# Performance work log

Hardware: AMD Instinct MI355X
Metric: run time of the kernel (lower is better)

## Reference

```python
import jax, jax.numpy as jnp
import numpy as np

B, K, H, T, V = 32, 5, 512, 256, 5000
MAX_LEN = 64
SOS, EOS, PAD = 1, 2, 0
NEG = -1e9
ALPHA, MIN_LEN = 1.2, 5.0
SCALE = 1.0 / float(np.sqrt(H))


def setup_inputs() -> dict:
    key = jax.random.key(0)
    ks = jax.random.split(key, 5)
    s = 0.02
    return {
        "input_var": jnp.full((B, 1), SOS, dtype=jnp.int32),
        "encoder_outputs": jax.random.normal(ks[0], (B, T, H), dtype=jnp.float32),
        "emb_table": jax.random.normal(ks[1], (V, H), dtype=jnp.float32) * s,
        "w_ih": jax.random.normal(ks[2], (H, 3 * H), dtype=jnp.float32) * s,
        "w_hh": jax.random.normal(ks[3], (H, 3 * H), dtype=jnp.float32) * s,
        "w_out": jax.random.normal(ks[4], (2 * H, V), dtype=jnp.float32) * s,
        "k": K,
    }


def _gru_cell(x, h, w_ih, w_hh):
    iz, ir, inn = jnp.split(x @ w_ih, 3, axis=-1)
    hz, hr, hn = jnp.split(h @ w_hh, 3, axis=-1)
    z = jax.nn.sigmoid(iz + hz)
    r = jax.nn.sigmoid(ir + hr)
    n = jnp.tanh(inn + r * hn)
    return (1.0 - z) * n + z * h


def _forward_step(tok, h, enc, emb_table, w_ih, w_hh, w_out):
    # tok: [N] int, h: [N,H], enc: [N,T,H] -> (log-probs [N,V], new hidden [N,H])
    x = emb_table[tok]
    h = _gru_cell(x, h, w_ih, w_hh)
    att = jax.nn.softmax(jnp.einsum("nh,nth->nt", h, enc) * SCALE, axis=-1)
    ctx = jnp.einsum("nt,nth->nh", att, enc)
    logits = jnp.concatenate([h, ctx], axis=-1) @ w_out
    return jax.nn.log_softmax(logits, axis=-1), h


def reference(input_var, encoder_outputs, emb_table, w_ih, w_hh, w_out, k):
    bsz = encoder_outputs.shape[0]
    f32 = encoder_outputs.dtype

    # --- first step on un-inflated batch (hidden starts at zeros) ---
    h0 = jnp.zeros((bsz, H), dtype=f32)
    lp0, h1 = _forward_step(input_var[:, 0], h0, encoder_outputs,
                            emb_table, w_ih, w_hh, w_out)
    cum, beams = jax.lax.top_k(lp0, k)            # [B,k], [B,k]

    # inflate encoder states / hidden to beam-major layout [B*k, ...]
    enc_k = jnp.repeat(encoder_outputs, k, axis=0)   # [B*k,T,H]
    h = jnp.repeat(h1, k, axis=0)                    # [B*k,H]

    tokens = jnp.zeros((bsz, k, MAX_LEN), dtype=jnp.int32)
    tokens = tokens.at[:, :, 0].set(beams)
    finished = beams == EOS
    lengths = jnp.ones((bsz, k), dtype=jnp.int32)
    # finished beams may only extend with PAD at zero added log-prob
    pad_lp = jnp.where(jnp.arange(V) == PAD, 0.0, NEG).astype(f32)

    def body(carry, di):
        tokens, last, cum, h, finished, lengths = carry
        lp, h_new = _forward_step(last.reshape(-1), h, enc_k,
                                  emb_table, w_ih, w_hh, w_out)
        lp = lp.reshape(bsz, k, V)
        lp = jnp.where(finished[:, :, None], pad_lp[None, None, :], lp)
        # joint top-k over k*V candidates == per-beam topk(k) then topk over k^2
        cand = (cum[:, :, None] + lp).reshape(bsz, k * V)
        scores, idx = jax.lax.top_k(cand, k)      # [B,k]
        beam_ids = idx // V
        tok_ids = idx % V
        tokens = jnp.take_along_axis(tokens, beam_ids[:, :, None], axis=1)
        tokens = tokens.at[:, :, di].set(tok_ids)
        prev_fin = jnp.take_along_axis(finished, beam_ids, axis=1)
        lengths = jnp.take_along_axis(lengths, beam_ids, axis=1) + jnp.where(prev_fin, 0, 1)
        finished = prev_fin | (tok_ids == EOS)
        h = jnp.take_along_axis(h_new.reshape(bsz, k, H),
                                beam_ids[:, :, None], axis=1).reshape(bsz * k, H)
        return (tokens, tok_ids, scores, h, finished, lengths), None

    carry = (tokens, beams.astype(jnp.int32), cum, h, finished, lengths)
    (tokens, _, cum, _, finished, lengths), _ = jax.lax.scan(
        body, carry, jnp.arange(1, MAX_LEN))

    # length penalty on finished hypotheses, then pick best beam per batch
    penalty = ((MIN_LEN + lengths.astype(f32)) / (MIN_LEN + 1.0)) ** ALPHA
    sel = jnp.where(finished, cum / penalty, cum)
    best = jnp.argmax(sel, axis=1)
    hypothesis = jnp.take_along_axis(tokens, best[:, None, None], axis=1)[:, 0, :]
    return hypothesis, cum
```

## Files before the change

### kernel.cpp

```cpp
#include <hip/hip_runtime.h>
#include <math.h>

#define BB     32
#define KBM    5
#define NR     160
#define HD     512
#define TT     256
#define VV     5000
#define MAXLEN 64
#define EOSID  2
#define NEGV   (-1e9f)
#define NEGBIG (-3.0e38f)
#define SCALEF 0.04419417382415922f
#define NBLK   256
#define NTHR   512

typedef float v4f __attribute__((ext_vector_type(4)));

__device__ __forceinline__ float ld_sysf(const float* p) {
  return __hip_atomic_load(p, __ATOMIC_RELAXED, __HIP_MEMORY_SCOPE_SYSTEM);
}
__device__ __forceinline__ void st_sysf(float* p, float v) {
  __hip_atomic_store(p, v, __ATOMIC_RELAXED, __HIP_MEMORY_SCOPE_SYSTEM);
}
__device__ __forceinline__ int ld_sysi(const int* p) {
  return __hip_atomic_load(p, __ATOMIC_RELAXED, __HIP_MEMORY_SCOPE_SYSTEM);
}
__device__ __forceinline__ void st_sysi(int* p, int v) {
  __hip_atomic_store(p, v, __ATOMIC_RELAXED, __HIP_MEMORY_SCOPE_SYSTEM);
}

__device__ __forceinline__ v4f ld4_issue_sys(const float* p) {
  v4f v;
  asm volatile("global_load_dwordx4 %0, %1, off sc0 sc1" : "=v"(v) : "v"(p));
  return v;
}
__device__ __forceinline__ v4f ld4_issue(const float* p) {
  v4f v;
  asm volatile("global_load_dwordx4 %0, %1, off" : "=v"(v) : "v"(p));
  return v;
}
__device__ __forceinline__ void vm_bind2(v4f& a, v4f& b) {
  asm volatile("s_waitcnt vmcnt(0)" : "+v"(a), "+v"(b) :: "memory");
}
__device__ __forceinline__ void vm_bind3(v4f& a, v4f& b, v4f& c) {
  asm volatile("s_waitcnt vmcnt(0)" : "+v"(a), "+v"(b), "+v"(c) :: "memory");
}
__device__ __forceinline__ void vm_bind4(v4f& a, v4f& b, v4f& c, v4f& d) {
  asm volatile("s_waitcnt vmcnt(0)" : "+v"(a), "+v"(b), "+v"(c), "+v"(d) :: "memory");
}
__device__ __forceinline__ void vm_bind5(v4f& a, v4f& b, v4f& c, v4f& d, v4f& e) {
  asm volatile("s_waitcnt vmcnt(0)"
               : "+v"(a), "+v"(b), "+v"(c), "+v"(d), "+v"(e) :: "memory");
}
__device__ __forceinline__ void st4_sys(float* p, v4f v) {
  asm volatile("global_store_dwordx4 %0, %1, off sc0 sc1" :: "v"(p), "v"(v) : "memory");
}

__device__ __forceinline__ bool viBetter(float av, int ai, float bv, int bi) {
  return (av > bv) || (av == bv && ai < bi);
}

__device__ __forceinline__ void top5_insert(float tv[5], int ti[5], float x, int v) {
  if (!viBetter(x, v, tv[4], ti[4])) return;
  tv[4] = x; ti[4] = v;
#pragma unroll
  for (int q = 4; q > 0; q--) {
    if (viBetter(tv[q], ti[q], tv[q - 1], ti[q - 1])) {
      float tf = tv[q - 1]; int tx2 = ti[q - 1];
      tv[q - 1] = tv[q]; ti[q - 1] = ti[q];
      tv[q] = tf; ti[q] = tx2;
    } else break;
  }
}

template<int LEVELS>
__device__ __forceinline__ void bfly_argmax(float& v, int& i) {
#pragma unroll
  for (int d = 1; d < (1 << LEVELS); d <<= 1) {
    float ov = __shfl_xor(v, d);
    int oi = __shfl_xor(i, d);
    if (viBetter(ov, oi, v, i)) { v = ov; i = oi; }
  }
}

__global__ void k_zero(unsigned int* bar) {
  if (threadIdx.x < 320)
    __hip_atomic_store(&bar[threadIdx.x], 0u, __ATOMIC_RELAXED, __HIP_MEMORY_SCOPE_SYSTEM);
}

__launch_bounds__(NTHR, 1)
__global__ void k_persist(const int* __restrict__ input_var, const float* __restrict__ enc,
                          const float* __restrict__ emb, const float* __restrict__ w_ih,
                          const float* __restrict__ w_hh, const float* __restrict__ w_out,
                          float* __restrict__ out,
                          float* h, float* A_cat, float* summ,
                          int* last_tok, unsigned int* bar) {
  const int bid = blockIdx.x;
  const int tid = threadIdx.x;
  unsigned int ep = 0;

  __shared__ float sh_xs[32][40];
  __shared__ float sh_hs[32][40];
  __shared__ float sh_ws[6][32][32];
  __shared__ int   sh_toks[32];
  __shared__ float sh_h5[KBM][HD];
  __shared__ float sh_part[2][KBM][TT];
  __shared__ float sh_sc5[KBM][TT];
  __shared__ float sh_tmp5[KBM][TT];
  __shared__ float sh_as[32][72];
  __shared__ float sh_bs[64][136];
  __shared__ float sh_candV[KBM * KBM]; __shared__ int sh_candI[KBM * KBM];
  __shared__ int   sh_tokens[KBM][MAXLEN];
  __shared__ float sh_cum[KBM];
  __shared__ int   sh_fin[KBM]; __shared__ int sh_len[KBM];
  __shared__ float sh_oc[KBM];  __shared__ int sh_ofin[KBM]; __shared__ int sh_olen[KBM];
  __shared__ int   sh_ttmp[KBM * MAXLEN];
  __shared__ int   sh_selI[KBM]; __shared__ float sh_selV[KBM];

  auto gbar = [&]() {
    asm volatile("s_waitcnt vmcnt(0)" ::: "memory");
    __syncthreads();
    ep += 1;
    if (tid == 0) {
      __hip_atomic_fetch_add(&bar[(bid & 7) * 32], 1u, __ATOMIC_RELAXED,
                             __HIP_MEMORY_SCOPE_SYSTEM);
      if (bid == 0) {
        for (int c = 0; c < 8; c++) {
          while (__hip_atomic_load(&bar[c * 32], __ATOMIC_RELAXED,
                                   __HIP_MEMORY_SCOPE_SYSTEM) < ep * 32u) {
            __builtin_amdgcn_s_sleep(1);
          }
        }
        __hip_atomic_store(&bar[288], ep, __ATOMIC_RELAXED, __HIP_MEMORY_SCOPE_SYSTEM);
      } else {
        while (__hip_atomic_load(&bar[288], __ATOMIC_RELAXED,
                                 __HIP_MEMORY_SCOPE_SYSTEM) < ep) {
          __builtin_amdgcn_s_sleep(2);
        }
      }
    }
    __syncthreads();
  };

  if (bid < BB) {
    if (tid < KBM) { sh_cum[tid] = 0.f; sh_fin[tid] = 0; sh_len[tid] = 0; }
    for (int t = tid; t < KBM * MAXLEN; t += NTHR) sh_tokens[t >> 6][t & 63] = 0;
  }
  {
    int gidx = bid * NTHR + tid;
    v4f z4; z4[0] = z4[1] = z4[2] = z4[3] = 0.f;
    for (int i = gidx; i < NR * HD / 4; i += NBLK * NTHR) st4_sys(&h[i * 4], z4);
    for (int t = gidx; t < NR; t += NBLK * NTHR) st_sysi(&last_tok[t], input_var[t / KBM]);
  }
  gbar();

  for (int di = 0; di < MAXLEN; di++) {
    if (bid < 80) {
      const int bx = bid & 15, by = bid >> 4;
      const int i0 = bx * 32, n0 = by * 32;
      const int tx = tid & 31, ty = tid >> 5;
      if (tid < 32) sh_toks[tid] = ld_sysi(&last_tok[n0 + tid]);
      float acc[6][2];
#pragma unroll
      for (int g = 0; g < 6; g++) { acc[g][0] = 0.f; acc[g][1] = 0.f; }
      float hcap0 = 0.f, hcap1 = 0.f;

      for (int k0 = 0; k0 < HD; k0 += 32) {
        __syncthreads();
        v4f v0, v1, v2, v3;
        if (tid < 256) {
          int r = tid >> 3, c4 = (tid & 7) * 4;
          v0 = ld4_issue(&emb[(size_t)sh_toks[r] * HD + k0 + c4]);
        } else {
          int r = (tid - 256) >> 3, c4 = ((tid - 256) & 7) * 4;
          v0 = ld4_issue_sys(&h[(size_t)(n0 + r) * HD + k0 + c4]);
        }
        int gW[3], kW[3], cW[3];
#pragma unroll
        for (int p = 0; p < 3; p++) {
          int widx = tid + p * 512;
          int g = widx >> 8, rem = widx & 255;
          int kk = rem >> 3, c4 = (rem & 7) * 4;
          const float* W = (g < 3) ? w_ih : w_hh;
          int gc = (g < 3) ? g : g - 3;
          v4f t = ld4_issue(&W[(size_t)(k0 + kk) * 1536 + gc * HD + i0 + c4]);
          if (p == 0) v1 = t; else if (p == 1) v2 = t; else v3 = t;
          gW[p] = g; kW[p] = kk; cW[p] = c4;
        }
        vm_bind4(v0, v1, v2, v3);
        if (tid < 256) {
          int r = tid >> 3, c4 = (tid & 7) * 4;
          *(v4f*)&sh_xs[r][c4] = v0;
        } else {
          int r = (tid - 256) >> 3, c4 = ((tid - 256) & 7) * 4;
          *(v4f*)&sh_hs[r][c4] = v0;
        }
        *(v4f*)&sh_ws[gW[0]][kW[0]][cW[0]] = v1;
        *(v4f*)&sh_ws[gW[1]][kW[1]][cW[1]] = v2;
        *(v4f*)&sh_ws[gW[2]][kW[2]][cW[2]] = v3;
        __syncthreads();
        if (k0 == i0) {
          hcap0 = sh_hs[ty * 2 + 0][tx];
          hcap1 = sh_hs[ty * 2 + 1][tx];
        }
#pragma unroll 8
        for (int k = 0; k < 32; k++) {
          float w0 = sh_ws[0][k][tx], w1 = sh_ws[1][k][tx], w2 = sh_ws[2][k][tx];
          float w3 = sh_ws[3][k][tx], w4 = sh_ws[4][k][tx], w5 = sh_ws[5][k][tx];
#pragma unroll
          for (int rr = 0; rr < 2; rr++) {
            float xv = sh_xs[ty * 2 + rr][k];
            float hv = sh_hs[ty * 2 + rr][k];
            acc[0][rr] += xv * w0; acc[1][rr] += xv * w1; acc[2][rr] += xv * w2;
            acc[3][rr] += hv * w3; acc[4][rr] += hv * w4; acc[5][rr] += hv * w5;
          }
        }
      }
#pragma unroll
      for (int rr = 0; rr < 2; rr++) {
        int n = n0 + ty * 2 + rr, i = i0 + tx;
        float hv = rr ? hcap1 : hcap0;
        float z = 1.f / (1.f + expf(-(acc[0][rr] + acc[3][rr])));
        float r = 1.f / (1.f + expf(-(acc[1][rr] + acc[4][rr])));
        float nn = tanhf(acc[2][rr] + r * acc[5][rr]);
        st_sysf(&A_cat[(size_t)n * 1024 + i], (1.f - z) * nn + z * hv);
      }
    }
    gbar();

    if (bid < BB) {
      const int b = bid;
      {
        v4f x0, x1 = {};
        int j0 = tid >> 7, kc0 = (tid & 127) * 4;
        x0 = ld4_issue_sys(&A_cat[(size_t)(b * KBM + j0) * 1024 + kc0]);
        if (tid < 128) {
          int idx = tid + 512;
          x1 = ld4_issue_sys(&A_cat[(size_t)(b * KBM + (idx >> 7)) * 1024 + (idx & 127) * 4]);
        }
        vm_bind2(x0, x1);
        *(v4f*)&sh_h5[j0][kc0] = x0;
        if (tid < 128) {
          int idx = tid + 512;
          *(v4f*)&sh_h5[idx >> 7][(idx & 127) * 4] = x1;
        }
      }
      __syncthreads();
      {
        const int t = tid & 255, half = tid >> 8;
        const int kb = half * 256;
        float a[KBM];
#pragma unroll
        for (int j = 0; j < KBM; j++) a[j] = 0.f;
        const float* ep2 = enc + ((size_t)b * TT + t) * HD + kb;
#pragma unroll 4
        for (int k = 0; k < 256; k += 4) {
          v4f e = *(const v4f*)(ep2 + k);
#pragma unroll
          for (int j = 0; j < KBM; j++) {
            v4f hj = *(const v4f*)&sh_h5[j][kb + k];
            a[j] += hj[0] * e[0] + hj[1] * e[1] + hj[2] * e[2] + hj[3] * e[3];
          }
        }
#pragma unroll
        for (int j = 0; j < KBM; j++) sh_part[half][j][t] = a[j];
      }
      __syncthreads();
      if (tid < 256) {
#pragma unroll
        for (int j = 0; j < KBM; j++) {
          float sc = (sh_part[0][j][tid] + sh_part[1][j][tid]) * SCALEF;
          sh_sc5[j][tid] = sc;
          sh_tmp5[j][tid] = sc;
        }
      }
      __syncthreads();
      for (int off = 128; off > 0; off >>= 1) {
        if (tid < off) {
#pragma unroll
          for (int j = 0; j < KBM; j++)
            sh_tmp5[j][tid] = fmaxf(sh_tmp5[j][tid], sh_tmp5[j][tid + off]);
        }
        __syncthreads();
      }
      float mj[KBM];
#pragma unroll
      for (int j = 0; j < KBM; j++) mj[j] = sh_tmp5[j][0];
      __syncthreads();
      if (tid < 256) {
#pragma unroll
        for (int j = 0; j < KBM; j++) {
          float e = expf(sh_sc5[j][tid] - mj[j]);
          sh_sc5[j][tid] = e;
          sh_tmp5[j][tid] = e;
        }
      }
      __syncthreads();
      for (int off = 128; off > 0; off >>= 1) {
        if (tid < off) {
#pragma unroll
          for (int j = 0; j < KBM; j++) sh_tmp5[j][tid] += sh_tmp5[j][tid + off];
        }
        __syncthreads();
      }
      float Sj[KBM];
#pragma unroll
      for (int j = 0; j < KBM; j++) Sj[j] = sh_tmp5[j][0];
      __syncthreads();
      if (tid < 256) {
#pragma unroll
        for (int j = 0; j < KBM; j++) sh_sc5[j][tid] = sh_sc5[j][tid] / Sj[j];
      }
      __syncthreads();
      {
        float cx[KBM];
#pragma unroll
        for (int j = 0; j < KBM; j++) cx[j] = 0.f;
        const float* eb = enc + (size_t)b * TT * HD + tid;
#pragma unroll 8
        for (int t2 = 0; t2 < TT; t2++) {
          float e = eb[(size_t)t2 * HD];
#pragma unroll
          for (int j = 0; j < KBM; j++) cx[j] += sh_sc5[j][t2] * e;
        }
#pragma unroll
        for (int j = 0; j < KBM; j++)
          st_sysf(&A_cat[(size_t)(b * KBM + j) * 1024 + HD + tid], cx[j]);
      }
    }
    gbar();

    if (bid < 200) {
      const int bc = bid % 40, br = bid / 40;
      const int c0 = bc * 128, n0 = br * 32;
      const int tx = tid & 31, ty = tid >> 5;
      float acc[2][4];
#pragma unroll
      for (int rr = 0; rr < 2; rr++)
#pragma unroll
        for (int cc = 0; cc < 4; cc++) acc[rr][cc] = 0.f;

      for (int k0 = 0; k0 < 1024; k0 += 64) {
        __syncthreads();
        v4f a0, b0, b1, b2, b3;
        const int ar = tid >> 4, ak4 = (tid & 15) * 4;
        a0 = ld4_issue_sys(&A_cat[(size_t)(n0 + ar) * 1024 + k0 + ak4]);
        int kkB[4], cB[4];
#pragma unroll
        for (int p = 0; p < 4; p++) {
          int idx = tid + p * 512;
          int kk = idx >> 5, c4 = (idx & 31) * 4;
          int col = c0 + c4;
          v4f t; t[0] = t[1] = t[2] = t[3] = 0.f;
          if (col + 3 < VV) t = ld4_issue(&w_out[(size_t)(k0 + kk) * VV + col]);
          if (p == 0) b0 = t; else if (p == 1) b1 = t; else if (p == 2) b2 = t; else b3 = t;
          kkB[p] = kk; cB[p] = c4;
        }
        vm_bind5(a0, b0, b1, b2, b3);
        *(v4f*)&sh_as[ar][ak4] = a0;
        *(v4f*)&sh_bs[kkB[0]][cB[0]] = b0;
        *(v4f*)&sh_bs[kkB[1]][cB[1]] = b1;
        *(v4f*)&sh_bs[kkB[2]][cB[2]] = b2;
        *(v4f*)&sh_bs[kkB[3]][cB[3]] = b3;
        __syncthreads();
#pragma unroll 16
        for (int k = 0; k < 64; k++) {
          v4f bv = *(const v4f*)&sh_bs[k][tx * 4];
#pragma unroll
          for (int rr = 0; rr < 2; rr++) {
            float a = sh_as[ty * 2 + rr][k];
            acc[rr][0] += a * bv[0]; acc[rr][1] += a * bv[1];
            acc[rr][2] += a * bv[2]; acc[rr][3] += a * bv[3];
          }
        }
      }
#pragma unroll
      for (int rr = 0; rr < 2; rr++) {
        const int rowg = n0 + ty * 2 + rr;
        float vv[4]; int ci[4];
        float m = NEGBIG, s = 0.f;
#pragma unroll
        for (int cc = 0; cc < 4; cc++) {
          int c = c0 + tx * 4 + cc;
          ci[cc] = c;
          if (c < VV) {
            float x = acc[rr][cc];
            vv[cc] = x;
            float mn = fmaxf(m, x);
            s = s * expf(m - mn) + expf(x - mn);
            m = mn;
          } else {
            vv[cc] = NEGBIG;
          }
        }
#pragma unroll
        for (int d = 1; d < 32; d <<= 1) {
          float om = __shfl_xor(m, d), os = __shfl_xor(s, d);
          float mm = fmaxf(m, om);
          s = s * expf(m - mm) + os * expf(om - mm);
          m = mm;
        }
        float tv[5]; int ti[5];
#pragma unroll
        for (int q = 0; q < 5; q++) {
          float bvv = vv[0]; int bii = ci[0];
#pragma unroll
          for (int cc = 1; cc < 4; cc++)
            if (viBetter(vv[cc], ci[cc], bvv, bii)) { bvv = vv[cc]; bii = ci[cc]; }
          bfly_argmax<5>(bvv, bii);
          tv[q] = bvv; ti[q] = bii;
#pragma unroll
          for (int cc = 0; cc < 4; cc++)
            if (ci[cc] == bii) vv[cc] = -3.2e38f;
        }
        if ((tid & 31) == 0) {
          float* base = &summ[((size_t)rowg * 40 + bc) * 12];
          v4f p0v, p1v, p2v;
          p0v[0] = m; p0v[1] = s; p0v[2] = tv[0]; p0v[3] = tv[1];
          p1v[0] = tv[2]; p1v[1] = tv[3]; p1v[2] = tv[4];
          p1v[3] = __int_as_float(ti[0]);
          p2v[0] = __int_as_float(ti[1]); p2v[1] = __int_as_float(ti[2]);
          p2v[2] = __int_as_float(ti[3]); p2v[3] = __int_as_float(ti[4]);
          st4_sys(base, p0v); st4_sys(base + 4, p1v); st4_sys(base + 8, p2v);
        }
      }
    }
    gbar();

    if (bid < BB) {
      const int b = bid;
      if (tid < KBM) {
        sh_oc[tid] = sh_cum[tid]; sh_ofin[tid] = sh_fin[tid]; sh_olen[tid] = sh_len[tid];
      }
      for (int t = tid; t < KBM * MAXLEN; t += NTHR) sh_ttmp[t] = sh_tokens[t >> 6][t & 63];
      __syncthreads();

      const int w = tid >> 6, lane = tid & 63;
      const bool act = (di == 0) ? (w == 0) : (w < KBM);
      if (act) {
        const int j = (di == 0) ? 0 : w;
        if (di > 0 && sh_ofin[j]) {
          if (lane == 0) {
            float cj = sh_oc[j];
            sh_candV[j * KBM + 0] = cj;
            sh_candI[j * KBM + 0] = j * VV + 0;
#pragma unroll
            for (int q = 1; q < KBM; q++) {
              sh_candV[j * KBM + q] = cj + NEGV;
              sh_candI[j * KBM + q] = j * VV + q;
            }
          }
        } else {
          const int row = b * KBM + j;
          float m, s; float lv[5]; int li[5];
          if (lane < 40) {
            const float* base = &summ[((size_t)row * 40 + lane) * 12];
            v4f s0 = ld4_issue_sys(base);
            v4f s1 = ld4_issue_sys(base + 4);
            v4f s2 = ld4_issue_sys(base + 8);
            vm_bind3(s0, s1, s2);
            m = s0[0]; s = s0[1];
            lv[0] = s0[2]; lv[1] = s0[3]; lv[2] = s1[0]; lv[3] = s1[1]; lv[4] = s1[2];
            li[0] = __float_as_int(s1[3]);
            li[1] = __float_as_int(s2[0]); li[2] = __float_as_int(s2[1]);
            li[3] = __float_as_int(s2[2]); li[4] = __float_as_int(s2[3]);
          } else {
            m = NEGBIG; s = 0.f;
#pragma unroll
            for (int q = 0; q < 5; q++) { lv[q] = NEGBIG; li[q] = 0x7fffffff; }
          }
#pragma unroll
          for (int d = 1; d < 64; d <<= 1) {
            float om = __shfl_xor(m, d), os = __shfl_xor(s, d);
            float mm = fmaxf(m, om);
            s = s * expf(m - mm) + os * expf(om - mm);
            m = mm;
          }
          float lse = m + logf(s);
          float cj = (di == 0) ? 0.f : sh_oc[j];
#pragma unroll
          for (int q = 0; q < 5; q++) {
            float bvv = lv[0]; int bii = li[0];
#pragma unroll
            for (int p = 1; p < 5; p++)
              if (viBetter(lv[p], li[p], bvv, bii)) { bvv = lv[p]; bii = li[p]; }
            bfly_argmax<6>(bvv, bii);
            if (lane == 0) {
              sh_candV[j * KBM + q] = cj + (bvv - lse);
              sh_candI[j * KBM + q] = j * VV + bii;
            }
#pragma unroll
            for (int p = 0; p < 5; p++)
              if (li[p] == bii) lv[p] = -3.2e38f;
          }
        }
      }
      __syncthreads();
      if (tid == 0) {
        if (di == 0) {
#pragma unroll
          for (int q = 0; q < KBM; q++) { sh_selV[q] = sh_candV[q]; sh_selI[q] = sh_candI[q]; }
        } else {
          float fv[5]; int fi[5];
#pragma unroll
          for (int q = 0; q < 5; q++) { fv[q] = -INFINITY; fi[q] = 0x7fffffff; }
          for (int t = 0; t < KBM * KBM; t++)
            top5_insert(fv, fi, sh_candV[t], sh_candI[t]);
#pragma unroll
          for (int q = 0; q < 5; q++) { sh_selV[q] = fv[q]; sh_selI[q] = fi[q]; }
        }
      }
      __syncthreads();
      if (tid < KBM) {
        int p = tid, idx = sh_selI[p];
        int bm = idx / VV, tk = idx - bm * VV;
        int pf = sh_ofin[bm];
        sh_cum[p] = sh_selV[p];
        sh_len[p] = sh_olen[bm] + (pf ? 0 : 1);
        sh_fin[p] = (pf || tk == EOSID) ? 1 : 0;
        st_sysi(&last_tok[b * KBM + p], tk);
      }
      for (int t = tid; t < KBM * MAXLEN; t += NTHR) {
        int p = t >> 6, pos = t & 63;
        int idx = sh_selI[p]; int bm = idx / VV; int tk = idx - bm * VV;
        sh_tokens[p][pos] = (pos == di) ? tk : sh_ttmp[bm * MAXLEN + pos];
      }
      __syncthreads();
      {
        int p0 = tid >> 7, e40 = (tid & 127) * 4;
        int bm0 = sh_selI[p0] / VV;
        v4f y0 = ld4_issue_sys(&A_cat[(size_t)(b * KBM + bm0) * 1024 + e40]);
        v4f y1 = {};
        if (tid < 128) {
          int bm1 = sh_selI[4] / VV;
          y1 = ld4_issue_sys(&A_cat[(size_t)(b * KBM + bm1) * 1024 + tid * 4]);
        }
        vm_bind2(y0, y1);
        st4_sys(&h[(size_t)(b * KBM + p0) * HD + e40], y0);
        if (tid < 128) st4_sys(&h[(size_t)(b * KBM + 4) * HD + tid * 4], y1);
      }
    }
    gbar();
  }

  if (bid < BB) {
    const int b = bid;
    if (tid == 0) {
      int best = 0; float bv = -INFINITY;
#pragma unroll
      for (int jj = 0; jj < KBM; jj++) {
        float c = sh_cum[jj];
        float pen = powf((5.0f + (float)sh_len[jj]) / 6.0f, 1.2f);
        float sel = sh_fin[jj] ? (c / pen) : c;
        if (sel > bv) { bv = sel; best = jj; }
      }
      sh_selI[0] = best;
    }
    __syncthreads();
    if (tid < MAXLEN) out[b * MAXLEN + tid] = (float)sh_tokens[sh_selI[0]][tid];
    if (tid < KBM) out[BB * MAXLEN + b * KBM + tid] = sh_cum[tid];
  }
}

extern "C" void kernel_launch(void* const* d_in, const int* in_sizes, int n_in,
                              void* d_out, int out_size, void* d_ws, size_t ws_size,
                              hipStream_t stream) {
  (void)in_sizes; (void)n_in; (void)out_size; (void)ws_size;
  const int*   input_var = (const int*)d_in[0];
  const float* enc       = (const float*)d_in[1];
  const float* emb       = (const float*)d_in[2];
  const float* w_ih      = (const float*)d_in[3];
  const float* w_hh      = (const float*)d_in[4];
  const float* w_out     = (const float*)d_in[5];
  float* out = (float*)d_out;

  float* h       = (float*)d_ws;
  float* A_cat   = h + (size_t)NR * HD;
  float* summ    = A_cat + (size_t)NR * 1024;
  int*   last_tok = (int*)(summ + (size_t)NR * 40 * 12);
  unsigned int* bar = (unsigned int*)(last_tok + NR);

  k_zero<<<1, 512, 0, stream>>>(bar);
  k_persist<<<NBLK, NTHR, 0, stream>>>(input_var, enc, emb, w_ih, w_hh, w_out, out,
                                       h, A_cat, summ, last_tok, bar);
}
```

Baseline: 9.458 ms.

## Ring-buffer A_cat per step, gather hidden via beam index, prefetch GEMM tiles

Replaces the single A_cat/h buffers with a 32-deep ring of per-step A buffers. The next GRU step gathers its hidden state directly from the previous buffer through a stored beam-selection index, which removes the explicit hidden-state reorder copy at the end of each step. Because buffers are no longer overwritten every step, loads switch from system-scope atomic loads to ordinary loads, with an acquire fence when the ring wraps. The GRU and output GEMM loops are software-pipelined so the next k-tile's global loads are issued while the current tile is computed. The cost is more workspace, and there is a risk of stale-cache reads through the non-coherent loads.

New measurement: 10.47 ms. +10.7%, slower.

```diff
diff --git a/kernel.cpp b/kernel.cpp
--- a/kernel.cpp
+++ b/kernel.cpp
@@ -14,6 +14,7 @@
 #define SCALEF 0.04419417382415922f
 #define NBLK   256
 #define NTHR   512
+#define NBUF   32
 
 typedef float v4f __attribute__((ext_vector_type(4)));
 
@@ -94,8 +95,8 @@
                           const float* __restrict__ emb, const float* __restrict__ w_ih,
                           const float* __restrict__ w_hh, const float* __restrict__ w_out,
                           float* __restrict__ out,
-                          float* h, float* A_cat, float* summ,
-                          int* last_tok, unsigned int* bar) {
+                          float* A_base, float* summ,
+                          int* last_tok, int* sel_bm, unsigned int* bar) {
   const int bid = blockIdx.x;
   const int tid = threadIdx.x;
   unsigned int ep = 0;
@@ -104,6 +105,7 @@
   __shared__ float sh_hs[32][40];
   __shared__ float sh_ws[6][32][32];
   __shared__ int   sh_toks[32];
+  __shared__ int   sh_srow[32];
   __shared__ float sh_h5[KBM][HD];
   __shared__ float sh_part[2][KBM][TT];
   __shared__ float sh_sc5[KBM][TT];
@@ -143,6 +145,8 @@
     __syncthreads();
   };
 
+  float* const A_zero = A_base + (size_t)NBUF * NR * 1024;
+
   if (bid < BB) {
     if (tid < KBM) { sh_cum[tid] = 0.f; sh_fin[tid] = 0; sh_len[tid] = 0; }
     for (int t = tid; t < KBM * MAXLEN; t += NTHR) sh_tokens[t >> 6][t & 63] = 0;
@@ -150,33 +154,43 @@
   {
     int gidx = bid * NTHR + tid;
     v4f z4; z4[0] = z4[1] = z4[2] = z4[3] = 0.f;
-    for (int i = gidx; i < NR * HD / 4; i += NBLK * NTHR) st4_sys(&h[i * 4], z4);
-    for (int t = gidx; t < NR; t += NBLK * NTHR) st_sysi(&last_tok[t], input_var[t / KBM]);
+    for (int i = gidx; i < NR * 1024 / 4; i += NBLK * NTHR) st4_sys(&A_zero[i * 4], z4);
+    for (int t = gidx; t < NR; t += NBLK * NTHR) {
+      st_sysi(&last_tok[t], input_var[t / KBM]);
+      st_sysi(&sel_bm[t], t % KBM);
+    }
   }
   gbar();
 
   for (int di = 0; di < MAXLEN; di++) {
+    float* A_cur = A_base + (size_t)(di & (NBUF - 1)) * NR * 1024;
+    const float* A_prev = (di == 0) ? A_zero
+                        : A_base + (size_t)((di - 1) & (NBUF - 1)) * NR * 1024;
+    if (di == NBUF) __builtin_amdgcn_fence(__ATOMIC_ACQUIRE, "agent");
+
     if (bid < 80) {
       const int bx = bid & 15, by = bid >> 4;
       const int i0 = bx * 32, n0 = by * 32;
       const int tx = tid & 31, ty = tid >> 5;
-      if (tid < 32) sh_toks[tid] = ld_sysi(&last_tok[n0 + tid]);
+      if (tid < 32) {
+        int n = n0 + tid;
+        sh_toks[tid] = ld_sysi(&last_tok[n]);
+        sh_srow[tid] = (n / KBM) * KBM + ld_sysi(&sel_bm[n]);
+      }
+      __syncthreads();
       float acc[6][2];
 #pragma unroll
       for (int g = 0; g < 6; g++) { acc[g][0] = 0.f; acc[g][1] = 0.f; }
       float hcap0 = 0.f, hcap1 = 0.f;
 
-      for (int k0 = 0; k0 < HD; k0 += 32) {
-        __syncthreads();
-        v4f v0, v1, v2, v3;
+      auto gru_issue = [&](int k0, v4f& q0, v4f& q1, v4f& q2, v4f& q3) {
         if (tid < 256) {
           int r = tid >> 3, c4 = (tid & 7) * 4;
-          v0 = ld4_issue(&emb[(size_t)sh_toks[r] * HD + k0 + c4]);
+          q0 = ld4_issue(&emb[(size_t)sh_toks[r] * HD + k0 + c4]);
         } else {
           int r = (tid - 256) >> 3, c4 = ((tid - 256) & 7) * 4;
-          v0 = ld4_issue_sys(&h[(size_t)(n0 + r) * HD + k0 + c4]);
-        }
-        int gW[3], kW[3], cW[3];
+          q0 = ld4_issue(&A_prev[(size_t)sh_srow[r] * 1024 + k0 + c4]);
+        }
 #pragma unroll
         for (int p = 0; p < 3; p++) {
           int widx = tid + p * 512;
@@ -185,20 +199,30 @@
           const float* W = (g < 3) ? w_ih : w_hh;
           int gc = (g < 3) ? g : g - 3;
           v4f t = ld4_issue(&W[(size_t)(k0 + kk) * 1536 + gc * HD + i0 + c4]);
-          if (p == 0) v1 = t; else if (p == 1) v2 = t; else v3 = t;
-          gW[p] = g; kW[p] = kk; cW[p] = c4;
-        }
-        vm_bind4(v0, v1, v2, v3);
+          if (p == 0) q1 = t; else if (p == 1) q2 = t; else q3 = t;
+        }
+      };
+
+      v4f c0v, c1v, c2v, c3v, d0v, d1v, d2v, d3v;
+      gru_issue(0, c0v, c1v, c2v, c3v);
+      for (int k0 = 0; k0 < HD; k0 += 32) {
+        vm_bind4(c0v, c1v, c2v, c3v);
+        __syncthreads();
         if (tid < 256) {
           int r = tid >> 3, c4 = (tid & 7) * 4;
-          *(v4f*)&sh_xs[r][c4] = v0;
+          *(v4f*)&sh_xs[r][c4] = c0v;
         } else {
           int r = (tid - 256) >> 3, c4 = ((tid - 256) & 7) * 4;
-          *(v4f*)&sh_hs[r][c4] = v0;
-        }
-        *(v4f*)&sh_ws[gW[0]][kW[0]][cW[0]] = v1;
-        *(v4f*)&sh_ws[gW[1]][kW[1]][cW[1]] = v2;
-        *(v4f*)&sh_ws[gW[2]][kW[2]][cW[2]] = v3;
+          *(v4f*)&sh_hs[r][c4] = c0v;
+        }
+#pragma unroll
+        for (int p = 0; p < 3; p++) {
+          int widx = tid + p * 512;
+          int g = widx >> 8, rem = widx & 255;
+          int kk = rem >> 3, c4 = (rem & 7) * 4;
+          *(v4f*)&sh_ws[g][kk][c4] = (p == 0) ? c1v : (p == 1) ? c2v : c3v;
+        }
+        if (k0 + 32 < HD) gru_issue(k0 + 32, d0v, d1v, d2v, d3v);
         __syncthreads();
         if (k0 == i0) {
           hcap0 = sh_hs[ty * 2 + 0][tx];
@@ -216,6 +240,7 @@
             acc[3][rr] += hv * w3; acc[4][rr] += hv * w4; acc[5][rr] += hv * w5;
           }
         }
+        c0v = d0v; c1v = d1v; c2v = d2v; c3v = d3v;
       }
 #pragma unroll
       for (int rr = 0; rr < 2; rr++) {
@@ -224,7 +249,7 @@
         float z = 1.f / (1.f + expf(-(acc[0][rr] + acc[3][rr])));
         float r = 1.f / (1.f + expf(-(acc[1][rr] + acc[4][rr])));
         float nn = tanhf(acc[2][rr] + r * acc[5][rr]);
-        st_sysf(&A_cat[(size_t)n * 1024 + i], (1.f - z) * nn + z * hv);
+        st_sysf(&A_cur[(size_t)n * 1024 + i], (1.f - z) * nn + z * hv);
       }
     }
     gbar();
@@ -234,10 +259,10 @@
       {
         v4f x0, x1 = {};
         int j0 = tid >> 7, kc0 = (tid & 127) * 4;
-        x0 = ld4_issue_sys(&A_cat[(size_t)(b * KBM + j0) * 1024 + kc0]);
+        x0 = ld4_issue(&A_cur[(size_t)(b * KBM + j0) * 1024 + kc0]);
         if (tid < 128) {
           int idx = tid + 512;
-          x1 = ld4_issue_sys(&A_cat[(size_t)(b * KBM + (idx >> 7)) * 1024 + (idx & 127) * 4]);
+          x1 = ld4_issue(&A_cur[(size_t)(b * KBM + (idx >> 7)) * 1024 + (idx & 127) * 4]);
         }
         vm_bind2(x0, x1);
         *(v4f*)&sh_h5[j0][kc0] = x0;
@@ -326,7 +351,7 @@
         }
 #pragma unroll
         for (int j = 0; j < KBM; j++)
-          st_sysf(&A_cat[(size_t)(b * KBM + j) * 1024 + HD + tid], cx[j]);
+          st_sysf(&A_cur[(size_t)(b * KBM + j) * 1024 + HD + tid], cx[j]);
       }
     }
     gbar();
@@ -341,12 +366,9 @@
 #pragma unroll
         for (int cc = 0; cc < 4; cc++) acc[rr][cc] = 0.f;
 
-      for (int k0 = 0; k0 < 1024; k0 += 64) {
-        __syncthreads();
-        v4f a0, b0, b1, b2, b3;
-        const int ar = tid >> 4, ak4 = (tid & 15) * 4;
-        a0 = ld4_issue_sys(&A_cat[(size_t)(n0 + ar) * 1024 + k0 + ak4]);
-        int kkB[4], cB[4];
+      auto gemm_issue = [&](int k0, v4f& qa, v4f& q0, v4f& q1, v4f& q2, v4f& q3) {
+        int ar = tid >> 4, ak4 = (tid & 15) * 4;
+        qa = ld4_issue(&A_cur[(size_t)(n0 + ar) * 1024 + k0 + ak4]);
 #pragma unroll
         for (int p = 0; p < 4; p++) {
           int idx = tid + p * 512;
@@ -354,15 +376,26 @@
           int col = c0 + c4;
           v4f t; t[0] = t[1] = t[2] = t[3] = 0.f;
           if (col + 3 < VV) t = ld4_issue(&w_out[(size_t)(k0 + kk) * VV + col]);
-          if (p == 0) b0 = t; else if (p == 1) b1 = t; else if (p == 2) b2 = t; else b3 = t;
-          kkB[p] = kk; cB[p] = c4;
-        }
+          if (p == 0) q0 = t; else if (p == 1) q1 = t; else if (p == 2) q2 = t; else q3 = t;
+        }
+      };
+
+      v4f a0, b0, b1, b2, b3, na, nb0, nb1, nb2, nb3;
+      gemm_issue(0, a0, b0, b1, b2, b3);
+      for (int k0 = 0; k0 < 1024; k0 += 64) {
         vm_bind5(a0, b0, b1, b2, b3);
-        *(v4f*)&sh_as[ar][ak4] = a0;
-        *(v4f*)&sh_bs[kkB[0]][cB[0]] = b0;
-        *(v4f*)&sh_bs[kkB[1]][cB[1]] = b1;
-        *(v4f*)&sh_bs[kkB[2]][cB[2]] = b2;
-        *(v4f*)&sh_bs[kkB[3]][cB[3]] = b3;
+        __syncthreads();
+        {
+          int ar = tid >> 4, ak4 = (tid & 15) * 4;
+          *(v4f*)&sh_as[ar][ak4] = a0;
+        }
+#pragma unroll
+        for (int p = 0; p < 4; p++) {
+          int idx = tid + p * 512;
+          int kk = idx >> 5, c4 = (idx & 31) * 4;
+          *(v4f*)&sh_bs[kk][c4] = (p == 0) ? b0 : (p == 1) ? b1 : (p == 2) ? b2 : b3;
+        }
+        if (k0 + 64 < 1024) gemm_issue(k0 + 64, na, nb0, nb1, nb2, nb3);
         __syncthreads();
 #pragma unroll 16
         for (int k = 0; k < 64; k++) {
@@ -374,6 +407,7 @@
             acc[rr][2] += a * bv[2]; acc[rr][3] += a * bv[3];
           }
         }
+        a0 = na; b0 = nb0; b1 = nb1; b2 = nb2; b3 = nb3;
       }
 #pragma unroll
       for (int rr = 0; rr < 2; rr++) {
@@ -520,25 +554,12 @@
         sh_len[p] = sh_olen[bm] + (pf ? 0 : 1);
         sh_fin[p] = (pf || tk == EOSID) ? 1 : 0;
         st_sysi(&last_tok[b * KBM + p], tk);
+        st_sysi(&sel_bm[b * KBM + p], bm);
       }
       for (int t = tid; t < KBM * MAXLEN; t += NTHR) {
         int p = t >> 6, pos = t & 63;
         int idx = sh_selI[p]; int bm = idx / VV; int tk = idx - bm * VV;
         sh_tokens[p][pos] = (pos == di) ? tk : sh_ttmp[bm * MAXLEN + pos];
-      }
-      __syncthreads();
-      {
-        int p0 = tid >> 7, e40 = (tid & 127) * 4;
-        int bm0 = sh_selI[p0] / VV;
-        v4f y0 = ld4_issue_sys(&A_cat[(size_t)(b * KBM + bm0) * 1024 + e40]);
-        v4f y1 = {};
-        if (tid < 128) {
-          int bm1 = sh_selI[4] / VV;
-          y1 = ld4_issue_sys(&A_cat[(size_t)(b * KBM + bm1) * 1024 + tid * 4]);
-        }
-        vm_bind2(y0, y1);
-        st4_sys(&h[(size_t)(b * KBM + p0) * HD + e40], y0);
-        if (tid < 128) st4_sys(&h[(size_t)(b * KBM + 4) * HD + tid * 4], y1);
       }
     }
     gbar();
@@ -575,13 +596,13 @@
   const float* w_out     = (const float*)d_in[5];
   float* out = (float*)d_out;
 
-  float* h       = (float*)d_ws;
-  float* A_cat   = h + (size_t)NR * HD;
-  float* summ    = A_cat + (size_t)NR * 1024;
+  float* A_base   = (float*)d_ws;
+  float* summ     = A_base + (size_t)(NBUF + 1) * NR * 1024;
   int*   last_tok = (int*)(summ + (size_t)NR * 40 * 12);
-  unsigned int* bar = (unsigned int*)(last_tok + NR);
+  int*   sel_bm   = last_tok + NR;
+  unsigned int* bar = (unsigned int*)(sel_bm + NR);
 
   k_zero<<<1, 512, 0, stream>>>(bar);
   k_persist<<<NBLK, NTHR, 0, stream>>>(input_var, enc, emb, w_ih, w_hh, w_out, out,
-                                       h, A_cat, summ, last_tok, bar);
-}
+                                       A_base, summ, last_tok, sel_bm, bar);
+}
```

## Overlap hidden-half of output GEMM with attention phase on separate blocks

Applied to the files above, without the earlier changes.

Splits the output-projection GEMM over K into the hidden half (k<512) and the context half. The hidden half now runs in blocks 0-199 during the attention phase, and attention moves to blocks 224-255. This lets GEMM work proceed before the grid barrier instead of leaving most blocks idle during attention. The remaining context half runs after the barrier, which shortens the critical path per decode step. It relies on 256 blocks being resident, and the accumulators now stay live across the barrier.

Result: faster. 8.159 ms (-13.7%).

```diff
diff --git a/kernel.cpp b/kernel.cpp
--- a/kernel.cpp
+++ b/kernel.cpp
@@ -229,8 +229,55 @@
     }
     gbar();
 
-    if (bid < BB) {
-      const int b = bid;
+    const bool isGemm = (bid < 200);
+    const int gbc = bid % 40;
+    const int gc0 = gbc * 128, gn0 = (bid / 40) * 32;
+    const int gtx = tid & 31, gty = tid >> 5;
+    float gacc[2][4];
+#pragma unroll
+    for (int rr = 0; rr < 2; rr++)
+#pragma unroll
+      for (int cc = 0; cc < 4; cc++) gacc[rr][cc] = 0.f;
+
+    auto gemm_chunk = [&](int k0) {
+      __syncthreads();
+      v4f a0, b0, b1, b2, b3;
+      const int ar = tid >> 4, ak4 = (tid & 15) * 4;
+      a0 = ld4_issue_sys(&A_cat[(size_t)(gn0 + ar) * 1024 + k0 + ak4]);
+      int kkB[4], cB[4];
+#pragma unroll
+      for (int p = 0; p < 4; p++) {
+        int idx = tid + p * 512;
+        int kk = idx >> 5, c4 = (idx & 31) * 4;
+        int col = gc0 + c4;
+        v4f t; t[0] = t[1] = t[2] = t[3] = 0.f;
+        if (col + 3 < VV) t = ld4_issue(&w_out[(size_t)(k0 + kk) * VV + col]);
+        if (p == 0) b0 = t; else if (p == 1) b1 = t; else if (p == 2) b2 = t; else b3 = t;
+        kkB[p] = kk; cB[p] = c4;
+      }
+      vm_bind5(a0, b0, b1, b2, b3);
+      *(v4f*)&sh_as[ar][ak4] = a0;
+      *(v4f*)&sh_bs[kkB[0]][cB[0]] = b0;
+      *(v4f*)&sh_bs[kkB[1]][cB[1]] = b1;
+      *(v4f*)&sh_bs[kkB[2]][cB[2]] = b2;
+      *(v4f*)&sh_bs[kkB[3]][cB[3]] = b3;
+      __syncthreads();
+#pragma unroll 16
+      for (int k = 0; k < 64; k++) {
+        v4f bv = *(const v4f*)&sh_bs[k][gtx * 4];
+#pragma unroll
+        for (int rr = 0; rr < 2; rr++) {
+          float a = sh_as[gty * 2 + rr][k];
+          gacc[rr][0] += a * bv[0]; gacc[rr][1] += a * bv[1];
+          gacc[rr][2] += a * bv[2]; gacc[rr][3] += a * bv[3];
+        }
+      }
+    };
+
+    if (isGemm) {
+      for (int k0 = 0; k0 < 512; k0 += 64) gemm_chunk(k0);
+    } else if (bid >= 224) {
+      const int b = bid - 224;
       {
         v4f x0, x1 = {};
         int j0 = tid >> 7, kc0 = (tid & 127) * 4;
@@ -331,61 +378,19 @@
     }
     gbar();
 
-    if (bid < 200) {
-      const int bc = bid % 40, br = bid / 40;
-      const int c0 = bc * 128, n0 = br * 32;
-      const int tx = tid & 31, ty = tid >> 5;
-      float acc[2][4];
-#pragma unroll
-      for (int rr = 0; rr < 2; rr++)
-#pragma unroll
-        for (int cc = 0; cc < 4; cc++) acc[rr][cc] = 0.f;
-
-      for (int k0 = 0; k0 < 1024; k0 += 64) {
-        __syncthreads();
-        v4f a0, b0, b1, b2, b3;
-        const int ar = tid >> 4, ak4 = (tid & 15) * 4;
-        a0 = ld4_issue_sys(&A_cat[(size_t)(n0 + ar) * 1024 + k0 + ak4]);
-        int kkB[4], cB[4];
-#pragma unroll
-        for (int p = 0; p < 4; p++) {
-          int idx = tid + p * 512;
-          int kk = idx >> 5, c4 = (idx & 31) * 4;
-          int col = c0 + c4;
-          v4f t; t[0] = t[1] = t[2] = t[3] = 0.f;
-          if (col + 3 < VV) t = ld4_issue(&w_out[(size_t)(k0 + kk) * VV + col]);
-          if (p == 0) b0 = t; else if (p == 1) b1 = t; else if (p == 2) b2 = t; else b3 = t;
-          kkB[p] = kk; cB[p] = c4;
-        }
-        vm_bind5(a0, b0, b1, b2, b3);
-        *(v4f*)&sh_as[ar][ak4] = a0;
-        *(v4f*)&sh_bs[kkB[0]][cB[0]] = b0;
-        *(v4f*)&sh_bs[kkB[1]][cB[1]] = b1;
-        *(v4f*)&sh_bs[kkB[2]][cB[2]] = b2;
-        *(v4f*)&sh_bs[kkB[3]][cB[3]] = b3;
-        __syncthreads();
-#pragma unroll 16
-        for (int k = 0; k < 64; k++) {
-          v4f bv = *(const v4f*)&sh_bs[k][tx * 4];
-#pragma unroll
-          for (int rr = 0; rr < 2; rr++) {
-            float a = sh_as[ty * 2 + rr][k];
-            acc[rr][0] += a * bv[0]; acc[rr][1] += a * bv[1];
-            acc[rr][2] += a * bv[2]; acc[rr][3] += a * bv[3];
-          }
-        }
-      }
+    if (isGemm) {
+      for (int k0 = 512; k0 < 1024; k0 += 64) gemm_chunk(k0);
 #pragma unroll
       for (int rr = 0; rr < 2; rr++) {
-        const int rowg = n0 + ty * 2 + rr;
+        const int rowg = gn0 + gty * 2 + rr;
         float vv[4]; int ci[4];
         float m = NEGBIG, s = 0.f;
 #pragma unroll
         for (int cc = 0; cc < 4; cc++) {
-          int c = c0 + tx * 4 + cc;
+          int c = gc0 + gtx * 4 + cc;
           ci[cc] = c;
           if (c < VV) {
-            float x = acc[rr][cc];
+            float x = gacc[rr][cc];
             vv[cc] = x;
             float mn = fmaxf(m, x);
             s = s * expf(m - mn) + expf(x - mn);
@@ -415,7 +420,7 @@
             if (ci[cc] == bii) vv[cc] = -3.2e38f;
         }
         if ((tid & 31) == 0) {
-          float* base = &summ[((size_t)rowg * 40 + bc) * 12];
+          float* base = &summ[((size_t)rowg * 40 + gbc) * 12];
           v4f p0v, p1v, p2v;
           p0v[0] = m; p0v[1] = s; p0v[2] = tv[0]; p0v[3] = tv[1];
           p1v[0] = tv[2]; p1v[1] = tv[3]; p1v[2] = tv[4];
```
